# Performance work log

Hardware: AMD Instinct MI355X
Metric: run time of the kernel (lower is better)

## Reference

```python
import jax, jax.numpy as jnp
import numpy as np

D = 3  # hardcoded window half-width in the module


def setup_inputs() -> dict:
    key = jax.random.key(0)
    ks = jax.random.split(key, 5)
    B, T, S = 16, 1024, 4096
    q_size, c_size, p_size = 512, 512, 512
    q = jax.random.normal(ks[0], (B, q_size, S), jnp.float32)
    c_t = jax.random.normal(ks[1], (B, T, c_size), jnp.float32)
    # torch nn.Linear weight layouts: (out_features, in_features)
    W_a = jax.random.normal(ks[2], (c_size, q_size), jnp.float32) / np.sqrt(q_size).astype(np.float32)
    W_p = jax.random.normal(ks[3], (p_size, c_size), jnp.float32) / np.sqrt(c_size).astype(np.float32)
    V_p = jax.random.normal(ks[4], (1, p_size), jnp.float32) / np.sqrt(p_size).astype(np.float32)
    return {"q": q, "c_t": c_t, "W_a": W_a, "W_p": W_p, "V_p": V_p}


def reference(q, c_t, W_a, W_p, V_p):
    B, q_size, S = q.shape
    # predictive alignment: p_t = S * sigmoid(V_p tanh(W_p c_t)) -> (B, T, 1)
    p_t = S * jax.nn.sigmoid(jnp.tanh(c_t @ W_p.T) @ V_p.T)
    # pad one NaN column at the front of the sequence, then (B, S+1, q_size)
    q_pad = jnp.pad(q, ((0, 0), (0, 0), (1, 0)), constant_values=jnp.nan).transpose(0, 2, 1)
    # window indices: clamp(long(p_t) + idx + 1, 0, S+1) % (S+1), idx in [-D, D]
    offsets = jnp.arange(-D + 1, D + 2)  # (2D+1,)
    s = jnp.clip(p_t.astype(jnp.int32) + offsets[None, None, :], 0, S + 1) % (S + 1)  # (B,T,2D+1)
    # per-batch gather of the local window: (B, T, 2D+1, q_size)
    qg = q_pad[jnp.arange(B)[:, None, None], s]
    nan_loc = jnp.isnan(qg[..., 0])  # (B, T, 2D+1)
    qg = jnp.where(nan_loc[..., None], 0.0, qg)
    # score: dot(W_a q, c_t) -> (B, T, 2D+1)
    a_t = jnp.einsum('btwq,cq,btc->btw', qg, W_a, c_t)
    a_t = jnp.where(nan_loc, -jnp.inf, a_t)
    attn = jax.nn.softmax(a_t, axis=2)
    # Gaussian decay around predicted position p_t
    gauss = jnp.exp(-2.0 * ((jnp.clip(s.astype(jnp.float32) - 1.0, 0.0, None) - p_t) / D) ** 2)
    W_attn = attn * gauss
    out = jnp.einsum('btw,btwq->btq', W_attn, qg)  # (B, T, q_size)
    return out
```

## Files before the change

### kernel.cpp

```cpp
#include <hip/hip_runtime.h>
#include <hip/hip_bf16.h>

#define BB 16
#define TT 1024
#define SS 4096
#define CS 512
#define QS 512
#define PS 512
#define NROW (BB*TT)

typedef unsigned short ushort_t;
typedef unsigned int u32;
typedef short bf16x8 __attribute__((ext_vector_type(8)));
typedef float f32x4 __attribute__((ext_vector_type(4)));

#define AS1 __attribute__((address_space(1)))
#define AS3 __attribute__((address_space(3)))

__device__ __forceinline__ void gl2l16(const void* g, void* l) {
    __builtin_amdgcn_global_load_lds((const AS1 u32*)g, (AS3 u32*)l, 16, 0, 0);
}

__device__ __forceinline__ ushort_t f2bf(float f) {
    u32 x = __float_as_uint(f);
    return (ushort_t)((x + 0x7fffu + ((x >> 16) & 1u)) >> 16);
}
__device__ __forceinline__ float bf2f(ushort_t b) {
    return __uint_as_float(((u32)b) << 16);
}

__global__ __launch_bounds__(256) void k_conv(const float* __restrict__ c,
                                              const float* __restrict__ Wa,
                                              const float* __restrict__ Wp,
                                              ushort_t* __restrict__ A,
                                              ushort_t* __restrict__ B,
                                              int* __restrict__ cnt) {
    const int blk = blockIdx.x;
    const int t = threadIdx.x;
    if (blk < 8192) {
        const int i = blk * 256 + t;
        const int m = i >> 7;
        const int k = (i & 127) * 4;
        float4 v = *(const float4*)(c + (size_t)m * CS + k);
        ushort4 hi, lo;
        hi.x = f2bf(v.x); lo.x = f2bf(v.x - bf2f(hi.x));
        hi.y = f2bf(v.y); lo.y = f2bf(v.y - bf2f(hi.y));
        hi.z = f2bf(v.z); lo.z = f2bf(v.z - bf2f(hi.z));
        hi.w = f2bf(v.w); lo.w = f2bf(v.w - bf2f(hi.w));
        *(ushort4*)(A + (size_t)m * 1024 + k)       = hi;
        *(ushort4*)(A + (size_t)m * 1024 + 512 + k) = lo;
    } else {
        const int n = blk - 8192;
        if (n == 0 && t < 2) cnt[t] = 0;
        #pragma unroll
        for (int kk = 0; kk < 2; ++kk) {
            const int k = t + 256 * kk;
            float v = (n < 512) ? Wa[(size_t)k * QS + n] : Wp[(size_t)(n - 512) * CS + k];
            ushort_t hi = f2bf(v);
            ushort_t lo = f2bf(v - bf2f(hi));
            B[(size_t)n * 1024 + k]       = hi;
            B[(size_t)n * 1024 + 512 + k] = lo;
        }
    }
}

__global__ __launch_bounds__(1024, 4) void k_gemm(const ushort_t* __restrict__ A,
                                                  const ushort_t* __restrict__ B,
                                                  const float* __restrict__ V_p,
                                                  const float* __restrict__ q,
                                                  float* __restrict__ qT,
                                                  float* __restrict__ u,
                                                  float* __restrict__ zpart) {
    __shared__ ushort_t lds[8][8192];
    const int tid = threadIdx.x;
    const int l = tid & 63;
    const int w = tid >> 6;
    const int wm = w >> 2;
    const int wn = w & 3;
    const int ln = l & 15, lh = l >> 4;

    const int orig = blockIdx.x;
    const int swz = ((orig & 7) << 5) + (orig >> 3);
    const int m0 = (swz >> 2) * 256;
    const int nt = swz & 3;
    const int n0 = nt * 256;

    const int srow = tid >> 2;
    const int scg  = tid & 3;
    const int scol0 = (scg ^ ((srow >> 1) & 3)) * 8;

    const int swzr = (lh ^ ((ln >> 1) & 3)) << 3;
    int aoffL[4], boffL[4];
    #pragma unroll
    for (int mi = 0; mi < 4; ++mi)
        aoffL[mi] = (wm * 64 + mi * 16 + ln) * 32 + swzr;
    #pragma unroll
    for (int ni = 0; ni < 4; ++ni)
        boffL[ni] = (wn * 64 + ni * 16 + ln) * 32 + swzr;

    const int tb = orig >> 4;
    const int sp = orig & 15;
    const int sq4 = sp * 256 + (((w & 3) << 4) + ln) * 4;
    const int dqb = ((w >> 2) << 5) + lh;
    float4 vq0, vq1, vq2, vq3;

    f32x4 acc[4][4];
    #pragma unroll
    for (int a = 0; a < 4; ++a)
        #pragma unroll
        for (int b2 = 0; b2 < 4; ++b2) acc[a][b2] = (f32x4){0.f, 0.f, 0.f, 0.f};

    auto STAGE = [&](int c) {
        const int tt = c >> 2, rem = c & 3, kh = rem >> 1;
        const int blk = tt >> 3, k0 = (tt & 7) << 6;
        const ushort_t* src;
        if (rem & 1) {
            const int boff = (blk == 1) ? 512 : 0;
            src = B + (size_t)(n0 + srow) * 1024 + boff + k0 + kh * 32 + scol0;
        } else {
            const int aoff = (blk == 2) ? 512 : 0;
            src = A + (size_t)(m0 + srow) * 1024 + aoff + k0 + kh * 32 + scol0;
        }
        gl2l16(src, &lds[c & 7][tid * 8]);
    };

    #pragma unroll
    for (int c = 0; c < 4; ++c) STAGE(c);
    asm volatile("s_waitcnt vmcnt(0)" ::: "memory");
    __builtin_amdgcn_s_barrier();

    #pragma unroll 1
    for (int t = 0; t < 24; ++t) {
        if (qT && t >= 1 && t <= 8) {
            const int d0 = (dqb + (t - 1) * 4) * 4;
            float* dst = qT + ((size_t)tb * SS + sq4) * QS + d0;
            *(float4*)(dst)          = make_float4(vq0.x, vq1.x, vq2.x, vq3.x);
            *(float4*)(dst + QS)     = make_float4(vq0.y, vq1.y, vq2.y, vq3.y);
            *(float4*)(dst + 2 * QS) = make_float4(vq0.z, vq1.z, vq2.z, vq3.z);
            *(float4*)(dst + 3 * QS) = make_float4(vq0.w, vq1.w, vq2.w, vq3.w);
        }
        if (t < 23) {
            #pragma unroll
            for (int i = 0; i < 4; ++i) STAGE(4 * t + 4 + i);
        }
        if (qT && t < 8) {
            const int d0 = (dqb + t * 4) * 4;
            const float* src = q + ((size_t)tb * QS + d0) * SS + sq4;
            vq0 = *(const float4*)(src);
            vq1 = *(const float4*)(src + SS);
            vq2 = *(const float4*)(src + 2 * SS);
            vq3 = *(const float4*)(src + 3 * SS);
        }
        {
            const ushort_t* bA = &lds[(4 * t) & 7][0];
            const ushort_t* bB = &lds[(4 * t + 1) & 7][0];
            bf16x8 af[4], bb[4];
            #pragma unroll
            for (int mi = 0; mi < 4; ++mi)
                af[mi] = *(const bf16x8*)(bA + aoffL[mi]);
            #pragma unroll
            for (int ni = 0; ni < 4; ++ni)
                bb[ni] = *(const bf16x8*)(bB + boffL[ni]);
            __builtin_amdgcn_s_setprio(1);
            #pragma unroll
            for (int mi = 0; mi < 4; ++mi)
                #pragma unroll
                for (int ni = 0; ni < 4; ++ni)
                    acc[mi][ni] = __builtin_amdgcn_mfma_f32_16x16x32_bf16(
                        af[mi], bb[ni], acc[mi][ni], 0, 0, 0);
            __builtin_amdgcn_s_setprio(0);
        }
        {
            const ushort_t* bA = &lds[(4 * t + 2) & 7][0];
            const ushort_t* bB = &lds[(4 * t + 3) & 7][0];
            bf16x8 af[4], bb[4];
            #pragma unroll
            for (int mi = 0; mi < 4; ++mi)
                af[mi] = *(const bf16x8*)(bA + aoffL[mi]);
            #pragma unroll
            for (int ni = 0; ni < 4; ++ni)
                bb[ni] = *(const bf16x8*)(bB + boffL[ni]);
            __builtin_amdgcn_s_setprio(1);
            #pragma unroll
            for (int mi = 0; mi < 4; ++mi)
                #pragma unroll
                for (int ni = 0; ni < 4; ++ni)
                    acc[mi][ni] = __builtin_amdgcn_mfma_f32_16x16x32_bf16(
                        af[mi], bb[ni], acc[mi][ni], 0, 0, 0);
            __builtin_amdgcn_s_setprio(0);
        }
        asm volatile("s_waitcnt vmcnt(0)" ::: "memory");
        __builtin_amdgcn_s_barrier();
    }

    if (nt < 2) {
        #pragma unroll
        for (int mi = 0; mi < 4; ++mi) {
            #pragma unroll
            for (int r = 0; r < 4; ++r) {
                const int m = m0 + wm * 64 + mi * 16 + lh * 4 + r;
                float* up = u + (size_t)m * QS + nt * 256 + wn * 64 + ln;
                #pragma unroll
                for (int ni = 0; ni < 4; ++ni) up[ni * 16] = acc[mi][ni][r];
            }
        }
    } else {
        float vp[4];
        #pragma unroll
        for (int ni = 0; ni < 4; ++ni)
            vp[ni] = V_p[(nt - 2) * 256 + wn * 64 + ni * 16 + ln];
        #pragma unroll
        for (int mi = 0; mi < 4; ++mi) {
            #pragma unroll
            for (int r = 0; r < 4; ++r) {
                float sv = 0.f;
                #pragma unroll
                for (int ni = 0; ni < 4; ++ni) sv += tanhf(acc[mi][ni][r]) * vp[ni];
                sv += __shfl_xor(sv, 1, 64);
                sv += __shfl_xor(sv, 2, 64);
                sv += __shfl_xor(sv, 4, 64);
                sv += __shfl_xor(sv, 8, 64);
                if (ln == 0)
                    zpart[(size_t)(m0 + wm * 64 + mi * 16 + lh * 4 + r) * 8 +
                          (nt - 2) * 4 + wn] = sv;
            }
        }
    }
}

__global__ __launch_bounds__(256) void k_z(const float* __restrict__ zpart,
                                           float* __restrict__ pt, int* __restrict__ tr,
                                           int* __restrict__ list1, int* __restrict__ cnt1) {
    const int row = blockIdx.x * 256 + threadIdx.x;
    const float4 a = *(const float4*)(zpart + (size_t)row * 8);
    const float4 b = *(const float4*)(zpart + (size_t)row * 8 + 4);
    float z = ((a.x + a.y) + (a.z + a.w)) + ((b.x + b.y) + (b.z + b.w));
    float ptv = 4096.f / (1.f + expf(-z));
    float fr = ptv - floorf(ptv);
    pt[row] = ptv;
    tr[row] = (int)ptv;
    if (fr < 0.06f || fr > 0.94f) {
        int i = atomicAdd(cnt1, 1);
        list1[i] = row;
    }
}

__global__ __launch_bounds__(256) void k_rep1(
    const float* __restrict__ c_t, const float* __restrict__ W_p,
    const float* __restrict__ V_p, float* __restrict__ pt, int* __restrict__ tr,
    const int* __restrict__ list1, const int* __restrict__ cnt1,
    int* __restrict__ list2, int* __restrict__ cnt2)
{
    const int tid = threadIdx.x;
    const int lane = tid & 63;
    const int wid = tid >> 6;
    const int n1 = cnt1[0];
    __shared__ float cl[8][132 * 4];
    __shared__ double zl[4][8];
    __shared__ int rows_s[8];

    for (int g0 = blockIdx.x * 8; g0 < n1; g0 += gridDim.x * 8) {
        const int nr = min(8, n1 - g0);
        __syncthreads();
        if (tid < nr) rows_s[tid] = list1[g0 + tid];
        __syncthreads();
        for (int idx = tid; idx < nr * 128; idx += 256) {
            int r = idx >> 7, k = (idx & 127) * 4;
            *(float4*)&cl[r][k] = *(const float4*)(c_t + (size_t)rows_s[r] * CS + k);
        }
        __syncthreads();

        const float* wp0 = W_p + (size_t)tid * CS;
        const float* wp1 = W_p + (size_t)(tid + 256) * CS;
        f32x4 acc[2][8];
        #pragma unroll
        for (int p = 0; p < 2; ++p)
            #pragma unroll
            for (int r = 0; r < 8; ++r) acc[p][r] = (f32x4){0.f, 0.f, 0.f, 0.f};

        for (int k = 0; k < CS; k += 16) {
            f32x4 w0[4], w1[4];
            #pragma unroll
            for (int j = 0; j < 4; ++j) {
                w0[j] = *(const f32x4*)(wp0 + k + 4 * j);
                w1[j] = *(const f32x4*)(wp1 + k + 4 * j);
            }
            #pragma unroll
            for (int j = 0; j < 4; ++j) {
                #pragma unroll
                for (int r = 0; r < 8; ++r) {
                    f32x4 c4 = *(const f32x4*)&cl[r][k + 4 * j];
                    acc[0][r] += c4 * w0[j];
                    acc[1][r] += c4 * w1[j];
                }
            }
        }

        const float vp0 = V_p[tid];
        const float vp1 = V_p[tid + 256];
        double zp[8];
        #pragma unroll
        for (int r = 0; r < 8; ++r) {
            float X0 = (acc[0][r][0] + acc[0][r][1]) + (acc[0][r][2] + acc[0][r][3]);
            float X1 = (acc[1][r][0] + acc[1][r][1]) + (acc[1][r][2] + acc[1][r][3]);
            zp[r] = (double)(tanhf(X0) * vp0) + (double)(tanhf(X1) * vp1);
        }
        #pragma unroll
        for (int r = 0; r < 8; ++r) {
            double v = zp[r];
            #pragma unroll
            for (int o = 32; o > 0; o >>= 1) v += __shfl_down(v, o, 64);
            if (lane == 0) zl[wid][r] = v;
        }
        __syncthreads();
        if (tid < nr) {
            double z = (zl[0][tid] + zl[1][tid]) + (zl[2][tid] + zl[3][tid]);
            double ptv = 4096.0 / (1.0 + exp(-z));
            const int row = rows_s[tid];
            pt[row] = (float)ptv;
            tr[row] = (int)ptv;
            double fr = ptv - floor(ptv);
            if (fr < 5e-3 || fr > 0.995) {
                int i2 = atomicAdd(cnt2, 1);
                list2[i2] = row;
            }
        }
    }
}

__global__ __launch_bounds__(256) void k_rep2a(
    const float* __restrict__ c_t, const float* __restrict__ W_p,
    const float* __restrict__ V_p,
    const int* __restrict__ list2, const int* __restrict__ cnt2,
    double* __restrict__ zp2)
{
    const int tid = threadIdx.x;
    const int pl = tid & 63;
    const int kq = tid >> 6;
    const int n2 = cnt2[0];
    __shared__ float cl[CS];
    __shared__ double xsh[4][64];

    for (int i = blockIdx.x; i < n2 * 8; i += gridDim.x) {
        const int li = i >> 3;
        const int pc = i & 7;
        const int row = list2[li];
        const int p0 = pc * 64;
        __syncthreads();
        if (tid < 128)
            *(float4*)(cl + tid * 4) = *(const float4*)(c_t + (size_t)row * CS + tid * 4);
        __syncthreads();
        const float* wr = W_p + (size_t)(p0 + pl) * CS + kq * 128;
        const float* cr = cl + kq * 128;
        double Xa = 0.0, Xb = 0.0, Xc = 0.0, Xd = 0.0;
        #pragma unroll 4
        for (int k = 0; k < 128; k += 4) {
            float4 w4 = *(const float4*)(wr + k);
            float4 c4 = *(const float4*)(cr + k);
            Xa += (double)c4.x * w4.x;
            Xb += (double)c4.y * w4.y;
            Xc += (double)c4.z * w4.z;
            Xd += (double)c4.w * w4.w;
        }
        xsh[kq][pl] = (Xa + Xb) + (Xc + Xd);
        __syncthreads();
        if (tid < 64) {
            double X = (xsh[0][pl] + xsh[1][pl]) + (xsh[2][pl] + xsh[3][pl]);
            double zv = tanh(X) * (double)V_p[p0 + pl];
            #pragma unroll
            for (int o = 32; o > 0; o >>= 1) zv += __shfl_down(zv, o, 64);
            if (pl == 0) zp2[i] = zv;
        }
    }
}

__global__ __launch_bounds__(256) void k_rep2b(
    const double* __restrict__ zp2, const int* __restrict__ list2,
    const int* __restrict__ cnt2, float* __restrict__ pt, int* __restrict__ tr)
{
    const int idx = blockIdx.x * 256 + threadIdx.x;
    if (idx >= cnt2[0]) return;
    const double* zr = zp2 + (size_t)idx * 8;
    double z = 0.0;
    #pragma unroll
    for (int j = 0; j < 8; ++j) z += zr[j];
    double ptv = 4096.0 / (1.0 + exp(-z));
    const int row = list2[idx];
    pt[row] = (float)ptv;
    tr[row] = (int)ptv;
}

__global__ __launch_bounds__(256) void k_attn_t(
    const float* __restrict__ qT, const float* __restrict__ u,
    const float* __restrict__ pt, const int* __restrict__ tr,
    float* __restrict__ out)
{
    const int wid = threadIdx.x >> 6;
    const int lane = threadIdx.x & 63;
    const int bt = blockIdx.x * 4 + wid;
    const int b = bt >> 10;

    const float* urow = u + (size_t)bt * QS;
    float4 ua = *(const float4*)(urow + lane * 8);
    float4 ub = *(const float4*)(urow + lane * 8 + 4);
    float uv[8] = {ua.x, ua.y, ua.z, ua.w, ub.x, ub.y, ub.z, ub.w};

    const float ptv = pt[bt];
    const int tn = tr[bt];
    const float* qTb = qT + (size_t)b * SS * QS;

    bool val[7];
    int pos[7];
    #pragma unroll
    for (int w = 0; w < 7; ++w) {
        int sv = tn + w - 2;
        sv = sv < 0 ? 0 : (sv > SS + 1 ? SS + 1 : sv);
        if (sv == SS + 1) sv = 0;
        val[w] = (sv != 0);
        pos[w] = sv - 1;
    }

    float qg[7][8];
    #pragma unroll
    for (int w = 0; w < 7; ++w) {
        if (val[w]) {
            const float* qr = qTb + (size_t)pos[w] * QS + lane * 8;
            float4 a = *(const float4*)qr;
            float4 c = *(const float4*)(qr + 4);
            qg[w][0] = a.x; qg[w][1] = a.y; qg[w][2] = a.z; qg[w][3] = a.w;
            qg[w][4] = c.x; qg[w][5] = c.y; qg[w][6] = c.z; qg[w][7] = c.w;
        } else {
            #pragma unroll
            for (int j = 0; j < 8; ++j) qg[w][j] = 0.f;
        }
    }

    float at[7];
    #pragma unroll
    for (int w = 0; w < 7; ++w) {
        float p = 0.f;
        #pragma unroll
        for (int j = 0; j < 8; ++j) p = fmaf(qg[w][j], uv[j], p);
        #pragma unroll
        for (int o = 1; o < 64; o <<= 1) p += __shfl_xor(p, o, 64);
        at[w] = p;
    }

    float m = -1e30f;
    #pragma unroll
    for (int w = 0; w < 7; ++w) if (val[w]) m = fmaxf(m, at[w]);
    float e[7], den = 0.f;
    #pragma unroll
    for (int w = 0; w < 7; ++w) { e[w] = val[w] ? expf(at[w] - m) : 0.f; den += e[w]; }
    const float inv = 1.f / den;

    float acc[8] = {0.f, 0.f, 0.f, 0.f, 0.f, 0.f, 0.f, 0.f};
    #pragma unroll
    for (int w = 0; w < 7; ++w) {
        if (val[w]) {
            float d = ((float)pos[w] - ptv) * (1.f / 3.f);
            float wt = e[w] * inv * expf(-2.f * d * d);
            #pragma unroll
            for (int j = 0; j < 8; ++j) acc[j] = fmaf(wt, qg[w][j], acc[j]);
        }
    }

    float* orow = out + (size_t)bt * QS + lane * 8;
    *(float4*)orow       = make_float4(acc[0], acc[1], acc[2], acc[3]);
    *(float4*)(orow + 4) = make_float4(acc[4], acc[5], acc[6], acc[7]);
}

__global__ __launch_bounds__(256) void k_attn_g(
    const float* __restrict__ q, const float* __restrict__ u,
    const float* __restrict__ pt, const int* __restrict__ tr,
    float* __restrict__ out)
{
    const int wid = threadIdx.x >> 6;
    const int lane = threadIdx.x & 63;
    const int bt = blockIdx.x * 4 + wid;
    const int b = bt >> 10;

    const float* urow = u + (size_t)bt * QS;
    float4 ua = *(const float4*)(urow + lane * 8);
    float4 ub = *(const float4*)(urow + lane * 8 + 4);
    float uv[8] = {ua.x, ua.y, ua.z, ua.w, ub.x, ub.y, ub.z, ub.w};

    const float ptv = pt[bt];
    const int tn = tr[bt];
    const float* qb = q + (size_t)b * QS * SS;

    bool val[7];
    int pos[7];
    #pragma unroll
    for (int w = 0; w < 7; ++w) {
        int sv = tn + w - 2;
        sv = sv < 0 ? 0 : (sv > SS + 1 ? SS + 1 : sv);
        if (sv == SS + 1) sv = 0;
        val[w] = (sv != 0);
        pos[w] = sv - 1;
    }

    float qg[7][8];
    #pragma unroll
    for (int j = 0; j < 8; ++j) {
        const float* qrow = qb + (size_t)(lane * 8 + j) * SS;
        #pragma unroll
        for (int w = 0; w < 7; ++w)
            qg[w][j] = val[w] ? qrow[pos[w]] : 0.f;
    }

    float at[7];
    #pragma unroll
    for (int w = 0; w < 7; ++w) {
        float p = 0.f;
        #pragma unroll
        for (int j = 0; j < 8; ++j) p = fmaf(qg[w][j], uv[j], p);
        #pragma unroll
        for (int o = 1; o < 64; o <<= 1) p += __shfl_xor(p, o, 64);
        at[w] = p;
    }

    float m = -1e30f;
    #pragma unroll
    for (int w = 0; w < 7; ++w) if (val[w]) m = fmaxf(m, at[w]);
    float e[7], den = 0.f;
    #pragma unroll
    for (int w = 0; w < 7; ++w) { e[w] = val[w] ? expf(at[w] - m) : 0.f; den += e[w]; }
    const float inv = 1.f / den;

    float acc[8] = {0.f, 0.f, 0.f, 0.f, 0.f, 0.f, 0.f, 0.f};
    #pragma unroll
    for (int w = 0; w < 7; ++w) {
        if (val[w]) {
            float d = ((float)pos[w] - ptv) * (1.f / 3.f);
            float wt = e[w] * inv * expf(-2.f * d * d);
            #pragma unroll
            for (int j = 0; j < 8; ++j) acc[j] = fmaf(wt, qg[w][j], acc[j]);
        }
    }

    float* orow = out + (size_t)bt * QS + lane * 8;
    *(float4*)orow       = make_float4(acc[0], acc[1], acc[2], acc[3]);
    *(float4*)(orow + 4) = make_float4(acc[4], acc[5], acc[6], acc[7]);
}

extern "C" void kernel_launch(void* const* d_in, const int* in_sizes, int n_in,
                              void* d_out, int out_size, void* d_ws, size_t ws_size,
                              hipStream_t stream) {
    const float* q   = (const float*)d_in[0];
    const float* c_t = (const float*)d_in[1];
    const float* W_a = (const float*)d_in[2];
    const float* W_p = (const float*)d_in[3];
    const float* V_p = (const float*)d_in[4];
    float* out = (float*)d_out;

    char* ws = (char*)d_ws;
    ushort_t* Ap  = (ushort_t*)(ws);
    ushort_t* Bp  = (ushort_t*)(ws + 33554432);
    float*    u   = (float*)  (ws + 35651584);
    float*    zp  = (float*)  (ws + 69206016);
    float*    pt  = (float*)  (ws + 69730304);
    int*      tr  = (int*)    (ws + 69795840);
    int*      l1  = (int*)    (ws + 69861376);
    int*      l2  = (int*)    (ws + 69926912);
    int*      cnt = (int*)    (ws + 69992448);
    double*   zp2 = (double*) (ws + 70000640);
    float*    qT  = (float*)  (ws + 73400320);
    const bool use_T = (ws_size >= 73400320ULL + 134217728ULL);

    hipLaunchKernelGGL(k_conv, dim3(9216), dim3(256), 0, stream,
                       c_t, W_a, W_p, Ap, Bp, cnt);
    hipLaunchKernelGGL(k_gemm, dim3(256), dim3(1024), 0, stream,
                       Ap, Bp, V_p, q, use_T ? qT : (float*)nullptr, u, zp);
    hipLaunchKernelGGL(k_z, dim3(64), dim3(256), 0, stream, zp, pt, tr, l1, cnt);
    hipLaunchKernelGGL(k_rep1, dim3(512), dim3(256), 0, stream,
                       c_t, W_p, V_p, pt, tr, l1, cnt, l2, cnt + 1);
    hipLaunchKernelGGL(k_rep2a, dim3(512), dim3(256), 0, stream,
                       c_t, W_p, V_p, l2, cnt + 1, zp2);
    hipLaunchKernelGGL(k_rep2b, dim3(64), dim3(256), 0, stream,
                       zp2, l2, cnt + 1, pt, tr);
    if (use_T)
        hipLaunchKernelGGL(k_attn_t, dim3(NROW / 4), dim3(256), 0, stream, qT, u, pt, tr, out);
    else
        hipLaunchKernelGGL(k_attn_g, dim3(NROW / 4), dim3(256), 0, stream, q, u, pt, tr, out);
}
```

Measured before the change: 248.6 us.

## Bucket rows by predicted position and gather q windows from LDS tiles

Removes the full q transpose that was written alongside the GEMM. Instead, rows are bucketed by batch and 32-wide position range using a histogram, scan and scatter. A new attention kernel loads only the q column tile for each bucket into shared memory, transposed, and serves every row in that bucket from it. This avoids writing and reading a 128MB transposed copy, at the cost of three extra small launches, atomics and possible load imbalance when many rows land in the same bucket.

```diff
diff --git a/kernel.cpp b/kernel.cpp
--- a/kernel.cpp
+++ b/kernel.cpp
@@ -34,7 +34,9 @@
                                               const float* __restrict__ Wp,
                                               ushort_t* __restrict__ A,
                                               ushort_t* __restrict__ B,
-                                              int* __restrict__ cnt) {
+                                              int* __restrict__ cnt,
+                                              int* __restrict__ hist,
+                                              int* __restrict__ cur) {
     const int blk = blockIdx.x;
     const int t = threadIdx.x;
     if (blk < 8192) {
@@ -49,7 +51,7 @@
         hi.w = f2bf(v.w); lo.w = f2bf(v.w - bf2f(hi.w));
         *(ushort4*)(A + (size_t)m * 1024 + k)       = hi;
         *(ushort4*)(A + (size_t)m * 1024 + 512 + k) = lo;
-    } else {
+    } else if (blk < 9216) {
         const int n = blk - 8192;
         if (n == 0 && t < 2) cnt[t] = 0;
         #pragma unroll
@@ -61,14 +63,16 @@
             B[(size_t)n * 1024 + k]       = hi;
             B[(size_t)n * 1024 + 512 + k] = lo;
         }
+    } else {
+        const int idx = (blk - 9216) * 256 + t;
+        if (idx < 2048) hist[idx] = 0;
+        else cur[idx - 2048] = 0;
     }
 }
 
 __global__ __launch_bounds__(1024, 4) void k_gemm(const ushort_t* __restrict__ A,
                                                   const ushort_t* __restrict__ B,
                                                   const float* __restrict__ V_p,
-                                                  const float* __restrict__ q,
-                                                  float* __restrict__ qT,
                                                   float* __restrict__ u,
                                                   float* __restrict__ zpart) {
     __shared__ ushort_t lds[8][8192];
@@ -97,12 +101,6 @@
     #pragma unroll
     for (int ni = 0; ni < 4; ++ni)
         boffL[ni] = (wn * 64 + ni * 16 + ln) * 32 + swzr;
-
-    const int tb = orig >> 4;
-    const int sp = orig & 15;
-    const int sq4 = sp * 256 + (((w & 3) << 4) + ln) * 4;
-    const int dqb = ((w >> 2) << 5) + lh;
-    float4 vq0, vq1, vq2, vq3;
 
     f32x4 acc[4][4];
     #pragma unroll
@@ -131,25 +129,9 @@
 
     #pragma unroll 1
     for (int t = 0; t < 24; ++t) {
-        if (qT && t >= 1 && t <= 8) {
-            const int d0 = (dqb + (t - 1) * 4) * 4;
-            float* dst = qT + ((size_t)tb * SS + sq4) * QS + d0;
-            *(float4*)(dst)          = make_float4(vq0.x, vq1.x, vq2.x, vq3.x);
-            *(float4*)(dst + QS)     = make_float4(vq0.y, vq1.y, vq2.y, vq3.y);
-            *(float4*)(dst + 2 * QS) = make_float4(vq0.z, vq1.z, vq2.z, vq3.z);
-            *(float4*)(dst + 3 * QS) = make_float4(vq0.w, vq1.w, vq2.w, vq3.w);
-        }
         if (t < 23) {
             #pragma unroll
             for (int i = 0; i < 4; ++i) STAGE(4 * t + 4 + i);
-        }
-        if (qT && t < 8) {
-            const int d0 = (dqb + t * 4) * 4;
-            const float* src = q + ((size_t)tb * QS + d0) * SS + sq4;
-            vq0 = *(const float4*)(src);
-            vq1 = *(const float4*)(src + SS);
-            vq2 = *(const float4*)(src + 2 * SS);
-            vq3 = *(const float4*)(src + 3 * SS);
         }
         {
             const ushort_t* bA = &lds[(4 * t) & 7][0];
@@ -390,158 +372,147 @@
     tr[row] = (int)ptv;
 }
 
-__global__ __launch_bounds__(256) void k_attn_t(
-    const float* __restrict__ qT, const float* __restrict__ u,
-    const float* __restrict__ pt, const int* __restrict__ tr,
-    float* __restrict__ out)
-{
-    const int wid = threadIdx.x >> 6;
-    const int lane = threadIdx.x & 63;
-    const int bt = blockIdx.x * 4 + wid;
-    const int b = bt >> 10;
-
-    const float* urow = u + (size_t)bt * QS;
-    float4 ua = *(const float4*)(urow + lane * 8);
-    float4 ub = *(const float4*)(urow + lane * 8 + 4);
-    float uv[8] = {ua.x, ua.y, ua.z, ua.w, ub.x, ub.y, ub.z, ub.w};
-
-    const float ptv = pt[bt];
-    const int tn = tr[bt];
-    const float* qTb = qT + (size_t)b * SS * QS;
-
-    bool val[7];
-    int pos[7];
-    #pragma unroll
-    for (int w = 0; w < 7; ++w) {
-        int sv = tn + w - 2;
-        sv = sv < 0 ? 0 : (sv > SS + 1 ? SS + 1 : sv);
-        if (sv == SS + 1) sv = 0;
-        val[w] = (sv != 0);
-        pos[w] = sv - 1;
-    }
-
-    float qg[7][8];
-    #pragma unroll
-    for (int w = 0; w < 7; ++w) {
-        if (val[w]) {
-            const float* qr = qTb + (size_t)pos[w] * QS + lane * 8;
-            float4 a = *(const float4*)qr;
-            float4 c = *(const float4*)(qr + 4);
-            qg[w][0] = a.x; qg[w][1] = a.y; qg[w][2] = a.z; qg[w][3] = a.w;
-            qg[w][4] = c.x; qg[w][5] = c.y; qg[w][6] = c.z; qg[w][7] = c.w;
-        } else {
-            #pragma unroll
-            for (int j = 0; j < 8; ++j) qg[w][j] = 0.f;
-        }
-    }
-
-    float at[7];
-    #pragma unroll
-    for (int w = 0; w < 7; ++w) {
-        float p = 0.f;
-        #pragma unroll
-        for (int j = 0; j < 8; ++j) p = fmaf(qg[w][j], uv[j], p);
-        #pragma unroll
-        for (int o = 1; o < 64; o <<= 1) p += __shfl_xor(p, o, 64);
-        at[w] = p;
-    }
-
-    float m = -1e30f;
-    #pragma unroll
-    for (int w = 0; w < 7; ++w) if (val[w]) m = fmaxf(m, at[w]);
-    float e[7], den = 0.f;
-    #pragma unroll
-    for (int w = 0; w < 7; ++w) { e[w] = val[w] ? expf(at[w] - m) : 0.f; den += e[w]; }
-    const float inv = 1.f / den;
-
-    float acc[8] = {0.f, 0.f, 0.f, 0.f, 0.f, 0.f, 0.f, 0.f};
-    #pragma unroll
-    for (int w = 0; w < 7; ++w) {
-        if (val[w]) {
-            float d = ((float)pos[w] - ptv) * (1.f / 3.f);
-            float wt = e[w] * inv * expf(-2.f * d * d);
-            #pragma unroll
-            for (int j = 0; j < 8; ++j) acc[j] = fmaf(wt, qg[w][j], acc[j]);
-        }
-    }
-
-    float* orow = out + (size_t)bt * QS + lane * 8;
-    *(float4*)orow       = make_float4(acc[0], acc[1], acc[2], acc[3]);
-    *(float4*)(orow + 4) = make_float4(acc[4], acc[5], acc[6], acc[7]);
-}
-
-__global__ __launch_bounds__(256) void k_attn_g(
+__global__ __launch_bounds__(256) void k_hist(const int* __restrict__ tr,
+                                              int* __restrict__ hist) {
+    const int row = blockIdx.x * 256 + threadIdx.x;
+    const int bucket = ((row >> 10) << 7) + (tr[row] >> 5);
+    atomicAdd(&hist[bucket], 1);
+}
+
+__global__ __launch_bounds__(1024) void k_scan(const int* __restrict__ hist,
+                                               int* __restrict__ offA) {
+    __shared__ int s0[1024], s1[1024];
+    const int t = threadIdx.x;
+    const int h0 = hist[2 * t];
+    const int h1 = hist[2 * t + 1];
+    s0[t] = h0 + h1;
+    __syncthreads();
+    int* src = s0;
+    int* dst = s1;
+    for (int off = 1; off < 1024; off <<= 1) {
+        int v = src[t] + ((t >= off) ? src[t - off] : 0);
+        dst[t] = v;
+        __syncthreads();
+        int* tmp = src; src = dst; dst = tmp;
+    }
+    const int excl = (t == 0) ? 0 : src[t - 1];
+    offA[2 * t]     = excl;
+    offA[2 * t + 1] = excl + h0;
+}
+
+__global__ __launch_bounds__(256) void k_scatter(const int* __restrict__ tr,
+                                                 const int* __restrict__ offA,
+                                                 int* __restrict__ cur,
+                                                 int* __restrict__ list) {
+    const int row = blockIdx.x * 256 + threadIdx.x;
+    const int bucket = ((row >> 10) << 7) + (tr[row] >> 5);
+    const int slot = atomicAdd(&cur[bucket], 1);
+    list[offA[bucket] + slot] = row;
+}
+
+__global__ __launch_bounds__(1024) void k_attn_f(
     const float* __restrict__ q, const float* __restrict__ u,
     const float* __restrict__ pt, const int* __restrict__ tr,
-    float* __restrict__ out)
+    const int* __restrict__ hist, const int* __restrict__ offA,
+    const int* __restrict__ list, float* __restrict__ out)
 {
-    const int wid = threadIdx.x >> 6;
-    const int lane = threadIdx.x & 63;
-    const int bt = blockIdx.x * 4 + wid;
-    const int b = bt >> 10;
-
-    const float* urow = u + (size_t)bt * QS;
-    float4 ua = *(const float4*)(urow + lane * 8);
-    float4 ub = *(const float4*)(urow + lane * 8 + 4);
-    float uv[8] = {ua.x, ua.y, ua.z, ua.w, ub.x, ub.y, ub.z, ub.w};
-
-    const float ptv = pt[bt];
-    const int tn = tr[bt];
+    const int bucket = blockIdx.x;
+    const int n = hist[bucket];
+    if (n == 0) return;
+    const int b = bucket >> 7;
+    const int c0 = (bucket & 127) << 5;
+    const int lo4 = (c0 >= 4) ? ((c0 - 3) & ~3) : 0;
+
+    __shared__ float tl[44 * 513];
+    const int tid = threadIdx.x;
     const float* qb = q + (size_t)b * QS * SS;
 
-    bool val[7];
-    int pos[7];
-    #pragma unroll
-    for (int w = 0; w < 7; ++w) {
-        int sv = tn + w - 2;
-        sv = sv < 0 ? 0 : (sv > SS + 1 ? SS + 1 : sv);
-        if (sv == SS + 1) sv = 0;
-        val[w] = (sv != 0);
-        pos[w] = sv - 1;
-    }
-
-    float qg[7][8];
-    #pragma unroll
-    for (int j = 0; j < 8; ++j) {
-        const float* qrow = qb + (size_t)(lane * 8 + j) * SS;
-        #pragma unroll
-        for (int w = 0; w < 7; ++w)
-            qg[w][j] = val[w] ? qrow[pos[w]] : 0.f;
-    }
-
-    float at[7];
-    #pragma unroll
-    for (int w = 0; w < 7; ++w) {
-        float p = 0.f;
-        #pragma unroll
-        for (int j = 0; j < 8; ++j) p = fmaf(qg[w][j], uv[j], p);
-        #pragma unroll
-        for (int o = 1; o < 64; o <<= 1) p += __shfl_xor(p, o, 64);
-        at[w] = p;
-    }
-
-    float m = -1e30f;
-    #pragma unroll
-    for (int w = 0; w < 7; ++w) if (val[w]) m = fmaxf(m, at[w]);
-    float e[7], den = 0.f;
-    #pragma unroll
-    for (int w = 0; w < 7; ++w) { e[w] = val[w] ? expf(at[w] - m) : 0.f; den += e[w]; }
-    const float inv = 1.f / den;
-
-    float acc[8] = {0.f, 0.f, 0.f, 0.f, 0.f, 0.f, 0.f, 0.f};
-    #pragma unroll
-    for (int w = 0; w < 7; ++w) {
-        if (val[w]) {
-            float d = ((float)pos[w] - ptv) * (1.f / 3.f);
-            float wt = e[w] * inv * expf(-2.f * d * d);
-            #pragma unroll
-            for (int j = 0; j < 8; ++j) acc[j] = fmaf(wt, qg[w][j], acc[j]);
-        }
-    }
-
-    float* orow = out + (size_t)bt * QS + lane * 8;
-    *(float4*)orow       = make_float4(acc[0], acc[1], acc[2], acc[3]);
-    *(float4*)(orow + 4) = make_float4(acc[4], acc[5], acc[6], acc[7]);
+    for (int idx = tid; idx < 512 * 11; idx += 1024) {
+        const int d = idx & 511;
+        const int c4 = idx >> 9;
+        const int s = lo4 + c4 * 4;
+        float4 v = make_float4(0.f, 0.f, 0.f, 0.f);
+        if (s + 3 <= SS - 1)
+            v = *(const float4*)(qb + (size_t)d * SS + s);
+        tl[(c4 * 4 + 0) * 513 + d] = v.x;
+        tl[(c4 * 4 + 1) * 513 + d] = v.y;
+        tl[(c4 * 4 + 2) * 513 + d] = v.z;
+        tl[(c4 * 4 + 3) * 513 + d] = v.w;
+    }
+    __syncthreads();
+
+    const int wv = tid >> 6;
+    const int l = tid & 63;
+    const int base = offA[bucket];
+
+    for (int wi = wv; wi < n; wi += 16) {
+        const int bt = list[base + wi];
+        const float ptv = pt[bt];
+        const int tn = tr[bt];
+
+        bool val[7];
+        int pos[7];
+        #pragma unroll
+        for (int w = 0; w < 7; ++w) {
+            int sv = tn + w - 2;
+            sv = sv < 0 ? 0 : (sv > SS + 1 ? SS + 1 : sv);
+            if (sv == SS + 1) sv = 0;
+            val[w] = (sv != 0);
+            pos[w] = sv - 1;
+        }
+
+        float uv[8];
+        #pragma unroll
+        for (int j = 0; j < 8; ++j)
+            uv[j] = u[(size_t)bt * QS + l + 64 * j];
+
+        float qg[7][8];
+        #pragma unroll
+        for (int w = 0; w < 7; ++w) {
+            if (val[w]) {
+                const float* tr0 = &tl[(pos[w] - lo4) * 513 + l];
+                #pragma unroll
+                for (int j = 0; j < 8; ++j) qg[w][j] = tr0[64 * j];
+            } else {
+                #pragma unroll
+                for (int j = 0; j < 8; ++j) qg[w][j] = 0.f;
+            }
+        }
+
+        float at[7];
+        #pragma unroll
+        for (int w = 0; w < 7; ++w) {
+            float p = 0.f;
+            #pragma unroll
+            for (int j = 0; j < 8; ++j) p = fmaf(qg[w][j], uv[j], p);
+            #pragma unroll
+            for (int o = 1; o < 64; o <<= 1) p += __shfl_xor(p, o, 64);
+            at[w] = p;
+        }
+
+        float m = -1e30f;
+        #pragma unroll
+        for (int w = 0; w < 7; ++w) if (val[w]) m = fmaxf(m, at[w]);
+        float e[7], den = 0.f;
+        #pragma unroll
+        for (int w = 0; w < 7; ++w) { e[w] = val[w] ? expf(at[w] - m) : 0.f; den += e[w]; }
+        const float inv = 1.f / den;
+
+        float acc[8] = {0.f, 0.f, 0.f, 0.f, 0.f, 0.f, 0.f, 0.f};
+        #pragma unroll
+        for (int w = 0; w < 7; ++w) {
+            if (val[w]) {
+                float d = ((float)pos[w] - ptv) * (1.f / 3.f);
+                float wt = e[w] * inv * expf(-2.f * d * d);
+                #pragma unroll
+                for (int j = 0; j < 8; ++j) acc[j] = fmaf(wt, qg[w][j], acc[j]);
+            }
+        }
+
+        #pragma unroll
+        for (int j = 0; j < 8; ++j)
+            out[(size_t)bt * QS + l + 64 * j] = acc[j];
+    }
 }
 
 extern "C" void kernel_launch(void* const* d_in, const int* in_sizes, int n_in,
@@ -555,23 +526,24 @@
     float* out = (float*)d_out;
 
     char* ws = (char*)d_ws;
-    ushort_t* Ap  = (ushort_t*)(ws);
-    ushort_t* Bp  = (ushort_t*)(ws + 33554432);
-    float*    u   = (float*)  (ws + 35651584);
-    float*    zp  = (float*)  (ws + 69206016);
-    float*    pt  = (float*)  (ws + 69730304);
-    int*      tr  = (int*)    (ws + 69795840);
-    int*      l1  = (int*)    (ws + 69861376);
-    int*      l2  = (int*)    (ws + 69926912);
-    int*      cnt = (int*)    (ws + 69992448);
-    double*   zp2 = (double*) (ws + 70000640);
-    float*    qT  = (float*)  (ws + 73400320);
-    const bool use_T = (ws_size >= 73400320ULL + 134217728ULL);
-
-    hipLaunchKernelGGL(k_conv, dim3(9216), dim3(256), 0, stream,
-                       c_t, W_a, W_p, Ap, Bp, cnt);
-    hipLaunchKernelGGL(k_gemm, dim3(256), dim3(1024), 0, stream,
-                       Ap, Bp, V_p, q, use_T ? qT : (float*)nullptr, u, zp);
+    ushort_t* Ap   = (ushort_t*)(ws);
+    ushort_t* Bp   = (ushort_t*)(ws + 33554432);
+    float*    u    = (float*)  (ws + 35651584);
+    float*    zp   = (float*)  (ws + 69206016);
+    float*    pt   = (float*)  (ws + 69730304);
+    int*      tr   = (int*)    (ws + 69795840);
+    int*      l1   = (int*)    (ws + 69861376);
+    int*      l2   = (int*)    (ws + 69926912);
+    int*      cnt  = (int*)    (ws + 69992448);
+    double*   zp2  = (double*) (ws + 69993472);
+    int*      hist = (int*)    (ws + 70124544);
+    int*      offA = (int*)    (ws + 70132736);
+    int*      cur  = (int*)    (ws + 70140928);
+    int*      list = (int*)    (ws + 70149120);
+
+    hipLaunchKernelGGL(k_conv, dim3(9232), dim3(256), 0, stream,
+                       c_t, W_a, W_p, Ap, Bp, cnt, hist, cur);
+    hipLaunchKernelGGL(k_gemm, dim3(256), dim3(1024), 0, stream, Ap, Bp, V_p, u, zp);
     hipLaunchKernelGGL(k_z, dim3(64), dim3(256), 0, stream, zp, pt, tr, l1, cnt);
     hipLaunchKernelGGL(k_rep1, dim3(512), dim3(256), 0, stream,
                        c_t, W_p, V_p, pt, tr, l1, cnt, l2, cnt + 1);
@@ -579,8 +551,9 @@
                        c_t, W_p, V_p, l2, cnt + 1, zp2);
     hipLaunchKernelGGL(k_rep2b, dim3(64), dim3(256), 0, stream,
                        zp2, l2, cnt + 1, pt, tr);
-    if (use_T)
-        hipLaunchKernelGGL(k_attn_t, dim3(NROW / 4), dim3(256), 0, stream, qT, u, pt, tr, out);
-    else
-        hipLaunchKernelGGL(k_attn_g, dim3(NROW / 4), dim3(256), 0, stream, q, u, pt, tr, out);
-}
+    hipLaunchKernelGGL(k_hist, dim3(64), dim3(256), 0, stream, tr, hist);
+    hipLaunchKernelGGL(k_scan, dim3(1), dim3(1024), 0, stream, hist, offA);
+    hipLaunchKernelGGL(k_scatter, dim3(64), dim3(256), 0, stream, tr, offA, cur, list);
+    hipLaunchKernelGGL(k_attn_f, dim3(2048), dim3(1024), 0, stream,
+                       q, u, pt, tr, hist, offA, list, out);
+}
```

New measurement: 228.4 us, median of 2. 1.09x faster.
